# Performance work log

Measured on AMD Instinct MI355X. Metric: run time of the kernel, lower is better.

The kernel has to match this reference:

```python
import jax, jax.numpy as jnp
import numpy as np

SOS = 1
EOS = 2


def setup_inputs() -> dict:
    key = jax.random.key(0)
    ks = jax.random.split(key, 8)
    B, Z, C, E, H, V = 64, 512, 512, 1024, 1024, 32000
    sc = 0.05  # small init so tanh/sigmoid stay in a sane range
    return {
        "zs": jax.random.normal(ks[0], (B, Z), jnp.float32),
        "cs": jax.random.normal(ks[1], (B, C), jnp.float32),
        "emb": jax.random.normal(ks[2], (V, E), jnp.float32) * sc,
        "W_ih": jax.random.normal(ks[3], (3 * H, E), jnp.float32) * sc,
        "W_hh": jax.random.normal(ks[4], (3 * H, H), jnp.float32) * sc,
        "b_ih": jnp.zeros((3 * H,), jnp.float32),
        "b_hh": jnp.zeros((3 * H,), jnp.float32),
        "W_out": jax.random.normal(ks[5], (V, H), jnp.float32) * sc,
        "b_out": jnp.zeros((V,), jnp.float32),
        "max_utt_len": 32,
    }


def _gru_cell(x, h, W_ih, W_hh, b_ih, b_hh):
    # PyTorch GRU cell math (single layer)
    gi = x @ W_ih.T + b_ih              # [B, 3H]
    gh = h @ W_hh.T + b_hh              # [B, 3H]
    i_r, i_z, i_n = jnp.split(gi, 3, axis=-1)
    h_r, h_z, h_n = jnp.split(gh, 3, axis=-1)
    r = jax.nn.sigmoid(i_r + h_r)
    z = jax.nn.sigmoid(i_z + h_z)
    n = jnp.tanh(i_n + r * h_n)
    return (1.0 - z) * n + z * h


def reference(zs, cs, emb, W_ih, W_hh, b_ih, b_hh, W_out, b_out, max_utt_len):
    B = zs.shape[0]
    h0 = jnp.concatenate([zs, cs], axis=1)       # [B, H] initial hidden (zcs)
    x0 = emb[jnp.full((B,), SOS)]                # embedded SOS tokens [B, E]

    def step(carry, _):
        x, h = carry
        h = _gru_cell(x, h, W_ih, W_hh, b_ih, b_hh)
        logits = h @ W_out.T + b_out             # [B, V]
        tok = jnp.argmax(logits, axis=-1)        # greedy decode
        return (emb[tok], h), tok

    (_, _), toks = jax.lax.scan(step, (x0, h0), None, length=max_utt_len)
    resps = toks.T.astype(jnp.int64)             # [B, T]

    # resp_lens: index of first EOS (with EOS appended) + 1
    eos = jnp.concatenate([resps == EOS, jnp.ones((B, 1), bool)], axis=1)
    resp_lens = jnp.argmax(eos, axis=1).astype(jnp.int64) + 1
    return resps, resp_lens
```

## Files before the change

kernel.cpp:

```cpp
#include <hip/hip_runtime.h>
#include <hip/hip_bf16.h>
#include <float.h>

#define NB 64
#define HD 1024
#define H3 3072
#define NC6 6144
#define NV 32000
#define TSTEPS 32
#define LBLK 500
#define BML 512
#define NSLICE 8
#define NKT 16
#define MARGIN_COEF 0.010f
#define MARGIN_ABS  1e-3f
#define MAXCAND 1024

using bf16x8 = __attribute__((ext_vector_type(8))) short;
using f32x4  = __attribute__((ext_vector_type(4))) float;
using s16x4  = __attribute__((ext_vector_type(4))) short;

#define SWZ(row, bo) ((((bo) & ~127)) | (((bo) & 112) ^ (((row) & 7) << 4)) | ((bo) & 15))

__device__ __forceinline__ void gl_lds16(const void* g, void* l) {
    __builtin_amdgcn_global_load_lds(
        (const __attribute__((address_space(1))) void*)g,
        (__attribute__((address_space(3))) void*)l, 16, 0, 0);
}
__device__ __forceinline__ float sigmoidf_(float x) {
    return 1.0f / (1.0f + expf(-x));
}
__device__ __forceinline__ float dot4(float4 h, float4 w, float a) {
    return fmaf(h.w, w.w, fmaf(h.z, w.z, fmaf(h.y, w.y, fmaf(h.x, w.x, a))));
}
__device__ __forceinline__ short bf16bits(float x) {
    __hip_bfloat16 b = __float2bfloat16(x);
    return __builtin_bit_cast(short, b);
}
__device__ __forceinline__ float bf16val(short s) {
    __hip_bfloat16 b = __builtin_bit_cast(__hip_bfloat16, s);
    return __bfloat162float(b);
}
__device__ __forceinline__ unsigned ordbits(float v) {
    unsigned u = __float_as_uint(v);
    return (u & 0x80000000u) ? ~u : (u | 0x80000000u);
}

__global__ __launch_bounds__(256) void wsplit2_kernel(
    const float* __restrict__ Wih, const float* __restrict__ Whh,
    short* __restrict__ WihSp, short* __restrict__ WhhSp)
{
    int r = blockIdx.x;
    const float* src = (r < H3) ? &Wih[(size_t)r * HD] : &Whh[(size_t)(r - H3) * HD];
    char* dst = (char*)((r < H3) ? &WihSp[(size_t)r * 2048] : &WhhSp[(size_t)(r - H3) * 2048]);
    int k = threadIdx.x * 4;
    float4 v = *(const float4*)&src[k];
    float xs[4] = {v.x, v.y, v.z, v.w};
    s16x4 p1, p2;
    #pragma unroll
    for (int e = 0; e < 4; ++e) {
        short s1 = bf16bits(xs[e]);
        short s2 = bf16bits(xs[e] - bf16val(s1));
        p1[e] = s1; p2[e] = s2;
    }
    int bo = k * 2;
    *(s16x4*)(dst + SWZ(r, bo))        = p1;
    *(s16x4*)(dst + SWZ(r, 2048 + bo)) = p2;
}

__global__ __launch_bounds__(256) void wbf_kernel(const float* __restrict__ W,
                                                  short* __restrict__ Wbf,
                                                  float* __restrict__ wnorm)
{
    int r = blockIdx.x, tdx = threadIdx.x;
    float4 v = *(const float4*)&W[(size_t)r * HD + tdx * 4];
    s16x4 p;
    p[0] = bf16bits(v.x); p[1] = bf16bits(v.y);
    p[2] = bf16bits(v.z); p[3] = bf16bits(v.w);
    char* dst = (char*)(Wbf + (size_t)r * HD);
    *(s16x4*)(dst + SWZ(r, tdx * 8)) = p;
    float ss = v.x*v.x + v.y*v.y + v.z*v.z + v.w*v.w;
    #pragma unroll
    for (int off = 32; off; off >>= 1) ss += __shfl_xor(ss, off);
    __shared__ float red[4];
    if ((tdx & 63) == 0) red[tdx >> 6] = ss;
    __syncthreads();
    if (tdx == 0) wnorm[r] = sqrtf(red[0] + red[1] + red[2] + red[3]);
}

__global__ __launch_bounds__(256) void init_kernel(
    const float* __restrict__ zs, const float* __restrict__ cs,
    const float* __restrict__ emb,
    float4* __restrict__ ht4, short* __restrict__ Hsp, short* __restrict__ Xsp,
    float* __restrict__ hnorm, unsigned long long* __restrict__ best)
{
    int b = blockIdx.x;
    int kg = threadIdx.x;
    int j = kg * 4;
    float4 v;
    if (j < 512) v = *(const float4*)&zs[b * 512 + j];
    else         v = *(const float4*)&cs[b * 512 + (j - 512)];
    ht4[kg * NB + b] = v;
    float hs[4] = {v.x, v.y, v.z, v.w};
    s16x4 p1, p2;
    #pragma unroll
    for (int e = 0; e < 4; ++e) {
        short s1 = bf16bits(hs[e]);
        short s2 = bf16bits(hs[e] - bf16val(s1));
        p1[e] = s1; p2[e] = s2;
    }
    int bo = j * 2;
    char* hdst = (char*)(Hsp + (size_t)b * 2048);
    *(s16x4*)(hdst + SWZ(b, bo))        = p1;
    *(s16x4*)(hdst + SWZ(b, 2048 + bo)) = p2;

    float4 x = *(const float4*)&emb[HD + j];
    float xs[4] = {x.x, x.y, x.z, x.w};
    #pragma unroll
    for (int e = 0; e < 4; ++e) {
        short s1 = bf16bits(xs[e]);
        short s2 = bf16bits(xs[e] - bf16val(s1));
        p1[e] = s1; p2[e] = s2;
    }
    char* xdst = (char*)(Xsp + (size_t)b * 2048);
    *(s16x4*)(xdst + SWZ(b, bo))        = p1;
    *(s16x4*)(xdst + SWZ(b, 2048 + bo)) = p2;

    float ss = hs[0]*hs[0] + hs[1]*hs[1] + hs[2]*hs[2] + hs[3]*hs[3];
    #pragma unroll
    for (int off = 32; off; off >>= 1) ss += __shfl_xor(ss, off);
    __shared__ float red[4];
    if ((kg & 63) == 0) red[kg >> 6] = ss;
    __syncthreads();
    if (kg == 0) {
        hnorm[b] = sqrtf(red[0] + red[1] + red[2] + red[3]);
        best[b] = 0ull;
    }
}

__global__ __launch_bounds__(256, 2) void gates_mfma(
    const short* __restrict__ Xsp, const short* __restrict__ Hsp,
    const short* __restrict__ WihSp, const short* __restrict__ WhhSp,
    float* __restrict__ gpart)
{
    __shared__ __align__(16) char tile[2][16384];

    const int tid = threadIdx.x;
    const int wv = tid >> 6, l = tid & 63;
    int cg = blockIdx.x >> 2;
    int ks = blockIdx.x & 3;
    int c0 = cg * 64;
    bool isH = c0 >= H3;
    const short* __restrict__ Asrc = isH ? Hsp : Xsp;
    const short* __restrict__ Wsrc = isH ? WhhSp : WihSp;
    int wc0 = c0 - (isH ? H3 : 0);
    int k0 = ks * 1024;
    int ka0 = (k0 & 1023) + (((k0 >> 10) & 1) << 10);
    int kw0 = (k0 & 1023) + ((k0 >> 11) << 10);

    const short* srows[4];
    int lof[4];
    #pragma unroll
    for (int i = 0; i < 4; ++i) {
        int slot = i * 256 + tid;
        int row = slot >> 3;
        int kb  = (slot & 7) * 16;
        const short* g = (row < 64)
            ? (Asrc + (size_t)row * 2048 + ka0)
            : (Wsrc + (size_t)(wc0 + row - 64) * 2048 + kw0);
        srows[i] = g + (kb >> 1);
        lof[i] = slot * 16;
    }

    int a_off[4][2], b_off[2];
    #pragma unroll
    for (int m = 0; m < 4; ++m)
        #pragma unroll
        for (int kf = 0; kf < 2; ++kf) {
            int row = m * 16 + (l & 15);
            int kb = kf * 64 + (l >> 4) * 16;
            a_off[m][kf] = row * 128 + (kb ^ ((row & 7) << 4));
        }
    #pragma unroll
    for (int kf = 0; kf < 2; ++kf) {
        int row = 64 + wv * 16 + (l & 15);
        int kb = kf * 64 + (l >> 4) * 16;
        b_off[kf] = row * 128 + (kb ^ ((row & 7) << 4));
    }

    f32x4 acc[4] = {};

    #pragma unroll
    for (int i = 0; i < 4; ++i) gl_lds16(srows[i], tile[0] + lof[i]);
    __syncthreads();

    int cur = 0;
    #pragma unroll 1
    for (int kt = 0; kt < NKT; ++kt) {
        if (kt + 1 < NKT) {
            #pragma unroll
            for (int i = 0; i < 4; ++i)
                gl_lds16(srows[i] + (size_t)(kt + 1) * 64, tile[cur ^ 1] + lof[i]);
        }
        char* buf = tile[cur];
        #pragma unroll
        for (int kf = 0; kf < 2; ++kf) {
            bf16x8 bfrag = *(const bf16x8*)(buf + b_off[kf]);
            #pragma unroll
            for (int m = 0; m < 4; ++m) {
                bf16x8 afrag = *(const bf16x8*)(buf + a_off[m][kf]);
                acc[m] = __builtin_amdgcn_mfma_f32_16x16x32_bf16(afrag, bfrag, acc[m], 0, 0, 0);
            }
        }
        __syncthreads();
        cur ^= 1;
    }

    int colw = c0 + wv * 16 + (l & 15);
    #pragma unroll
    for (int m = 0; m < 4; ++m)
        #pragma unroll
        for (int j = 0; j < 4; ++j) {
            int row = m * 16 + (l >> 4) * 4 + j;
            gpart[(size_t)(ks * NB + row) * NC6 + colw] = acc[m][j];
        }
}

__global__ __launch_bounds__(256) void gru_fuse(
    const float* __restrict__ gpart,
    const float* __restrict__ bih, const float* __restrict__ bhh,
    float4* __restrict__ ht4, short* __restrict__ Hsp,
    float* __restrict__ hnorm, unsigned long long* __restrict__ best)
{
    int b = blockIdx.x;
    int kg = threadIdx.x;
    int j0 = kg * 4;
    float4 ir = {}, iz = {}, in_ = {}, hr = {}, hz = {}, hn = {};
    #pragma unroll
    for (int ks = 0; ks < 4; ++ks) {
        const float* g = gpart + (size_t)(ks * NB + b) * NC6;
        float4 a;
        a = *(const float4*)&g[j0];             ir.x+=a.x; ir.y+=a.y; ir.z+=a.z; ir.w+=a.w;
        a = *(const float4*)&g[HD + j0];        iz.x+=a.x; iz.y+=a.y; iz.z+=a.z; iz.w+=a.w;
        a = *(const float4*)&g[2*HD + j0];      in_.x+=a.x; in_.y+=a.y; in_.z+=a.z; in_.w+=a.w;
        a = *(const float4*)&g[H3 + j0];        hr.x+=a.x; hr.y+=a.y; hr.z+=a.z; hr.w+=a.w;
        a = *(const float4*)&g[H3 + HD + j0];   hz.x+=a.x; hz.y+=a.y; hz.z+=a.z; hz.w+=a.w;
        a = *(const float4*)&g[H3 + 2*HD + j0]; hn.x+=a.x; hn.y+=a.y; hn.z+=a.z; hn.w+=a.w;
    }
    float4 vbi0 = *(const float4*)&bih[j0];
    float4 vbi1 = *(const float4*)&bih[HD + j0];
    float4 vbi2 = *(const float4*)&bih[2*HD + j0];
    float4 vbh0 = *(const float4*)&bhh[j0];
    float4 vbh1 = *(const float4*)&bhh[HD + j0];
    float4 vbh2 = *(const float4*)&bhh[2*HD + j0];
    float4 hv = ht4[kg * NB + b];
    float irv[4] = {ir.x+vbi0.x, ir.y+vbi0.y, ir.z+vbi0.z, ir.w+vbi0.w};
    float izv[4] = {iz.x+vbi1.x, iz.y+vbi1.y, iz.z+vbi1.z, iz.w+vbi1.w};
    float inv[4] = {in_.x+vbi2.x, in_.y+vbi2.y, in_.z+vbi2.z, in_.w+vbi2.w};
    float hrv[4] = {hr.x+vbh0.x, hr.y+vbh0.y, hr.z+vbh0.z, hr.w+vbh0.w};
    float hzv[4] = {hz.x+vbh1.x, hz.y+vbh1.y, hz.z+vbh1.z, hz.w+vbh1.w};
    float hnv[4] = {hn.x+vbh2.x, hn.y+vbh2.y, hn.z+vbh2.z, hn.w+vbh2.w};
    float hvv[4] = {hv.x, hv.y, hv.z, hv.w};
    float o[4];
    #pragma unroll
    for (int u = 0; u < 4; ++u) {
        float r = sigmoidf_(irv[u] + hrv[u]);
        float z = sigmoidf_(izv[u] + hzv[u]);
        float n = tanhf(inv[u] + r * hnv[u]);
        o[u] = (1.0f - z) * n + z * hvv[u];
    }
    ht4[kg * NB + b] = make_float4(o[0], o[1], o[2], o[3]);

    s16x4 p1, p2;
    #pragma unroll
    for (int e = 0; e < 4; ++e) {
        short s1 = bf16bits(o[e]);
        short s2 = bf16bits(o[e] - bf16val(s1));
        p1[e] = s1; p2[e] = s2;
    }
    int bo = j0 * 2;
    char* hdst = (char*)(Hsp + (size_t)b * 2048);
    *(s16x4*)(hdst + SWZ(b, bo))        = p1;
    *(s16x4*)(hdst + SWZ(b, 2048 + bo)) = p2;

    float ss = o[0]*o[0] + o[1]*o[1] + o[2]*o[2] + o[3]*o[3];
    #pragma unroll
    for (int off = 32; off; off >>= 1) ss += __shfl_xor(ss, off);
    __shared__ float red[4];
    if ((kg & 63) == 0) red[kg >> 6] = ss;
    __syncthreads();
    if (kg == 0) {
        hnorm[b] = sqrtf(red[0] + red[1] + red[2] + red[3]);
        best[b] = 0ull;
    }
}

__global__ __launch_bounds__(256, 2) void logits_lb(
    const short* __restrict__ Hsp, const short* __restrict__ Wbf,
    const float* __restrict__ bout, const float* __restrict__ wnorm,
    const float* __restrict__ hnorm,
    float* __restrict__ lb, float* __restrict__ bmlow)
{
    __shared__ __align__(16) char tile[2][16384];
    __shared__ float smax[64][4];

    const int tid = threadIdx.x;
    const int wv = tid >> 6, l = tid & 63;
    const int blk = blockIdx.x;

    const short* srows[4];
    int lof[4];
    #pragma unroll
    for (int i = 0; i < 4; ++i) {
        int slot = i * 256 + tid;
        int row = slot >> 3;
        int kb  = (slot & 7) * 16;
        const short* g = (row < 64)
            ? (Hsp + (size_t)row * 2048)
            : (Wbf + ((size_t)(blk * 64 + (row - 64))) * HD);
        srows[i] = g + (kb >> 1);
        lof[i] = slot * 16;
    }

    int a_off[4][2], b_off[2];
    #pragma unroll
    for (int m = 0; m < 4; ++m)
        #pragma unroll
        for (int kf = 0; kf < 2; ++kf) {
            int row = m * 16 + (l & 15);
            int kb = kf * 64 + (l >> 4) * 16;
            a_off[m][kf] = row * 128 + (kb ^ ((row & 7) << 4));
        }
    #pragma unroll
    for (int kf = 0; kf < 2; ++kf) {
        int row = 64 + wv * 16 + (l & 15);
        int kb = kf * 64 + (l >> 4) * 16;
        b_off[kf] = row * 128 + (kb ^ ((row & 7) << 4));
    }

    f32x4 acc[4] = {};

    #pragma unroll
    for (int i = 0; i < 4; ++i) gl_lds16(srows[i], tile[0] + lof[i]);
    __syncthreads();

    int cur = 0;
    #pragma unroll 1
    for (int kt = 0; kt < NKT; ++kt) {
        if (kt + 1 < NKT) {
            #pragma unroll
            for (int i = 0; i < 4; ++i)
                gl_lds16(srows[i] + (size_t)(kt + 1) * 64, tile[cur ^ 1] + lof[i]);
        }
        char* buf = tile[cur];
        #pragma unroll
        for (int kf = 0; kf < 2; ++kf) {
            bf16x8 bfrag = *(const bf16x8*)(buf + b_off[kf]);
            #pragma unroll
            for (int m = 0; m < 4; ++m) {
                bf16x8 afrag = *(const bf16x8*)(buf + a_off[m][kf]);
                acc[m] = __builtin_amdgcn_mfma_f32_16x16x32_bf16(afrag, bfrag, acc[m], 0, 0, 0);
            }
        }
        __syncthreads();
        cur ^= 1;
    }

    int col = blk * 64 + wv * 16 + (l & 15);
    float bo = bout[col];
    float wn = wnorm[col];
    float selmax = -FLT_MAX;
    int pick = l & 15;
    #pragma unroll
    for (int m = 0; m < 4; ++m) {
        #pragma unroll
        for (int j = 0; j < 4; ++j) {
            int row = m * 16 + (l >> 4) * 4 + j;
            float lbv = acc[m][j] + bo;
            lb[(size_t)row * NV + col] = lbv;
            float low = lbv - (MARGIN_COEF * hnorm[row] * wn + MARGIN_ABS);
            #pragma unroll
            for (int mask = 1; mask <= 8; mask <<= 1)
                low = fmaxf(low, __shfl_xor(low, mask, 64));
            if (pick == m * 4 + j) selmax = low;
        }
    }
    int row = ((l & 15) >> 2) * 16 + (l >> 4) * 4 + (l & 3);
    smax[row][wv] = selmax;
    __syncthreads();
    if (wv == 0) {
        float v = fmaxf(fmaxf(smax[l][0], smax[l][1]), fmaxf(smax[l][2], smax[l][3]));
        bmlow[(size_t)l * BML + blk] = v;
    }
}

__global__ __launch_bounds__(256) void select2_kernel(
    const float* __restrict__ lb, const float* __restrict__ wnorm,
    const float* __restrict__ hnorm, const float* __restrict__ bmlow,
    const float* __restrict__ Wout, const float* __restrict__ bout,
    const float4* __restrict__ ht4,
    unsigned long long* __restrict__ best)
{
    int b = blockIdx.x >> 3, slice = blockIdx.x & 7;
    int tid = threadIdx.x, wv = tid >> 6;
    const float* lbr = lb + (size_t)b * NV;
    float coef = MARGIN_COEF * hnorm[b];

    __shared__ int scount;
    __shared__ int cand[MAXCAND];
    __shared__ float tred[4];
    if (tid == 0) scount = 0;

    float tv = -FLT_MAX;
    for (int i = tid; i < LBLK; i += 256) tv = fmaxf(tv, bmlow[(size_t)b * BML + i]);
    #pragma unroll
    for (int off = 32; off; off >>= 1) tv = fmaxf(tv, __shfl_xor(tv, off));
    if ((tid & 63) == 0) tred[wv] = tv;
    __syncthreads();
    float tb = fmaxf(fmaxf(tred[0], tred[1]), fmaxf(tred[2], tred[3]));

    int c0 = slice * (NV / NSLICE);
    for (int c = c0 + tid; c < c0 + NV / NSLICE; c += 256) {
        if (lbr[c] + (coef * wnorm[c] + MARGIN_ABS) >= tb) {
            int s = atomicAdd(&scount, 1);
            if (s < MAXCAND) cand[s] = c;
        }
    }
    __syncthreads();
    int n = scount < MAXCAND ? scount : MAXCAND;
    if (n == 0) return;

    float4 h4 = ht4[tid * NB + b];
    __shared__ float rsum[4];
    for (int s = 0; s < n; ++s) {
        int c = cand[s];
        float4 w4 = *(const float4*)&Wout[(size_t)c * HD + tid * 4];
        float p = dot4(h4, w4, 0.0f);
        #pragma unroll
        for (int off = 32; off; off >>= 1) p += __shfl_xor(p, off);
        if ((tid & 63) == 0) rsum[wv] = p;
        __syncthreads();
        if (tid == 0) {
            float tot = rsum[0] + rsum[1] + rsum[2] + rsum[3] + bout[c];
            unsigned long long key =
                ((unsigned long long)ordbits(tot) << 32) | (unsigned)(~c);
            atomicMax(&best[b], key);
        }
        __syncthreads();
    }
}

__global__ __launch_bounds__(256) void gather_kernel(
    const unsigned long long* __restrict__ best,
    const float* __restrict__ emb, int* __restrict__ resps, int t,
    short* __restrict__ Xsp)
{
    int b = blockIdx.x, tid = threadIdx.x;
    int c = ~(unsigned)(best[b] & 0xFFFFFFFFull);
    if (tid == 0) resps[b * TSTEPS + t] = c;
    int k = tid * 4;
    float4 e = *(const float4*)&emb[(size_t)c * HD + k];
    float xs[4] = {e.x, e.y, e.z, e.w};
    s16x4 p1, p2;
    #pragma unroll
    for (int u = 0; u < 4; ++u) {
        short s1 = bf16bits(xs[u]);
        short s2 = bf16bits(xs[u] - bf16val(s1));
        p1[u] = s1; p2[u] = s2;
    }
    int bo = k * 2;
    char* xdst = (char*)(Xsp + (size_t)b * 2048);
    *(s16x4*)(xdst + SWZ(b, bo))        = p1;
    *(s16x4*)(xdst + SWZ(b, 2048 + bo)) = p2;
}

__global__ void resp_lens_kernel(const int* __restrict__ resps, int* __restrict__ lens)
{
    int b = threadIdx.x;
    if (b >= NB) return;
    int len = TSTEPS + 1;
    for (int t = TSTEPS - 1; t >= 0; t--)
        if (resps[b * TSTEPS + t] == 2) len = t + 1;
    lens[b] = len;
}

extern "C" void kernel_launch(void* const* d_in, const int* in_sizes, int n_in,
                              void* d_out, int out_size, void* d_ws, size_t ws_size,
                              hipStream_t stream) {
    const float* zs   = (const float*)d_in[0];
    const float* cs   = (const float*)d_in[1];
    const float* emb  = (const float*)d_in[2];
    const float* Wih  = (const float*)d_in[3];
    const float* Whh  = (const float*)d_in[4];
    const float* bih  = (const float*)d_in[5];
    const float* bhh  = (const float*)d_in[6];
    const float* Wout = (const float*)d_in[7];
    const float* bout = (const float*)d_in[8];
    int* out = (int*)d_out;

    char* ws = (char*)d_ws;
    float4* ht4  = (float4*)ws; ws += (size_t)256 * NB * 16;
    float*  gpart = (float*)ws; ws += (size_t)4 * NB * NC6 * 4;
    short*  Hsp  = (short*)ws;  ws += (size_t)NB * 2048 * 2;
    short*  Xsp  = (short*)ws;  ws += (size_t)NB * 2048 * 2;
    float*  wnorm = (float*)ws; ws += (size_t)NV * 4;
    float*  hnorm = (float*)ws; ws += 256;
    float*  bmlow = (float*)ws; ws += (size_t)NB * BML * 4;
    unsigned long long* best = (unsigned long long*)ws; ws += NB * 8;
    float*  lb   = (float*)ws;  ws += (size_t)NB * NV * 4;
    short*  Wbf  = (short*)ws;  ws += (size_t)NV * HD * 2;
    short*  WihSp = (short*)ws; ws += (size_t)H3 * 2048 * 2;
    short*  WhhSp = (short*)ws; ws += (size_t)H3 * 2048 * 2;

    wsplit2_kernel<<<NC6, 256, 0, stream>>>(Wih, Whh, WihSp, WhhSp);
    wbf_kernel<<<NV, 256, 0, stream>>>(Wout, Wbf, wnorm);
    init_kernel<<<NB, 256, 0, stream>>>(zs, cs, emb, ht4, Hsp, Xsp, hnorm, best);
    for (int t = 0; t < TSTEPS; t++) {
        gates_mfma<<<96 * 4, 256, 0, stream>>>(Xsp, Hsp, WihSp, WhhSp, gpart);
        gru_fuse<<<NB, 256, 0, stream>>>(gpart, bih, bhh, ht4, Hsp, hnorm, best);
        logits_lb<<<LBLK, 256, 0, stream>>>(Hsp, Wbf, bout, wnorm, hnorm, lb, bmlow);
        select2_kernel<<<NB * NSLICE, 256, 0, stream>>>(lb, wnorm, hnorm, bmlow,
                                                        Wout, bout, ht4, best);
        gather_kernel<<<NB, 256, 0, stream>>>(best, emb, out, t, Xsp);
    }
    resp_lens_kernel<<<1, 64, 0, stream>>>(out, out + NB * TSTEPS);
}
```

Measured before the change: 1.599 ms.

## Deepen MFMA load pipeline to 3 stages and fuse gather into select

The two MFMA GEMM kernels move from a double-buffered LDS tile with two barriers per k-step to a four-slot ring that prefetches two tiles ahead. Each step now has a single explicit vmcnt wait plus barrier, so global loads get more time to overlap with compute. Separately, the per-step gather kernel is removed. The last select block for each batch row, found by an atomic done counter, reads the winning token, writes the response and builds the next split-bf16 embedding input. This trades an extra LDS footprint per block and some fence/atomic overhead for fewer launches and less load stall.

```diff
diff --git a/kernel.cpp b/kernel.cpp
--- a/kernel.cpp
+++ b/kernel.cpp
@@ -46,6 +46,12 @@
     return (u & 0x80000000u) ? ~u : (u | 0x80000000u);
 }
 
+#define WAIT_BARRIER(kt) do { \
+    if ((kt) < NKT - 2)       asm volatile("s_waitcnt vmcnt(8)\ns_barrier" ::: "memory"); \
+    else if ((kt) == NKT - 2) asm volatile("s_waitcnt vmcnt(4)\ns_barrier" ::: "memory"); \
+    else                      asm volatile("s_waitcnt vmcnt(0)\ns_barrier" ::: "memory"); \
+} while (0)
+
 __global__ __launch_bounds__(256) void wsplit2_kernel(
     const float* __restrict__ Wih, const float* __restrict__ Whh,
     short* __restrict__ WihSp, short* __restrict__ WhhSp)
@@ -92,7 +98,8 @@
     const float* __restrict__ zs, const float* __restrict__ cs,
     const float* __restrict__ emb,
     float4* __restrict__ ht4, short* __restrict__ Hsp, short* __restrict__ Xsp,
-    float* __restrict__ hnorm, unsigned long long* __restrict__ best)
+    float* __restrict__ hnorm, unsigned long long* __restrict__ best,
+    int* __restrict__ done)
 {
     int b = blockIdx.x;
     int kg = threadIdx.x;
@@ -135,6 +142,7 @@
     if (kg == 0) {
         hnorm[b] = sqrtf(red[0] + red[1] + red[2] + red[3]);
         best[b] = 0ull;
+        done[b] = 0;
     }
 }
 
@@ -143,7 +151,7 @@
     const short* __restrict__ WihSp, const short* __restrict__ WhhSp,
     float* __restrict__ gpart)
 {
-    __shared__ __align__(16) char tile[2][16384];
+    __shared__ __align__(16) char tile[4][16384];
 
     const int tid = threadIdx.x;
     const int wv = tid >> 6, l = tid & 63;
@@ -192,17 +200,18 @@
 
     #pragma unroll
     for (int i = 0; i < 4; ++i) gl_lds16(srows[i], tile[0] + lof[i]);
-    __syncthreads();
-
-    int cur = 0;
+    #pragma unroll
+    for (int i = 0; i < 4; ++i) gl_lds16(srows[i] + 64, tile[1] + lof[i]);
+
     #pragma unroll 1
     for (int kt = 0; kt < NKT; ++kt) {
-        if (kt + 1 < NKT) {
+        if (kt + 2 < NKT) {
             #pragma unroll
             for (int i = 0; i < 4; ++i)
-                gl_lds16(srows[i] + (size_t)(kt + 1) * 64, tile[cur ^ 1] + lof[i]);
-        }
-        char* buf = tile[cur];
+                gl_lds16(srows[i] + (size_t)(kt + 2) * 64, tile[(kt + 2) & 3] + lof[i]);
+        }
+        WAIT_BARRIER(kt);
+        const char* buf = tile[kt & 3];
         #pragma unroll
         for (int kf = 0; kf < 2; ++kf) {
             bf16x8 bfrag = *(const bf16x8*)(buf + b_off[kf]);
@@ -212,8 +221,6 @@
                 acc[m] = __builtin_amdgcn_mfma_f32_16x16x32_bf16(afrag, bfrag, acc[m], 0, 0, 0);
             }
         }
-        __syncthreads();
-        cur ^= 1;
     }
 
     int colw = c0 + wv * 16 + (l & 15);
@@ -230,7 +237,8 @@
     const float* __restrict__ gpart,
     const float* __restrict__ bih, const float* __restrict__ bhh,
     float4* __restrict__ ht4, short* __restrict__ Hsp,
-    float* __restrict__ hnorm, unsigned long long* __restrict__ best)
+    float* __restrict__ hnorm, unsigned long long* __restrict__ best,
+    int* __restrict__ done)
 {
     int b = blockIdx.x;
     int kg = threadIdx.x;
@@ -292,6 +300,7 @@
     if (kg == 0) {
         hnorm[b] = sqrtf(red[0] + red[1] + red[2] + red[3]);
         best[b] = 0ull;
+        done[b] = 0;
     }
 }
 
@@ -301,7 +310,7 @@
     const float* __restrict__ hnorm,
     float* __restrict__ lb, float* __restrict__ bmlow)
 {
-    __shared__ __align__(16) char tile[2][16384];
+    __shared__ __align__(16) char tile[4][16384];
     __shared__ float smax[64][4];
 
     const int tid = threadIdx.x;
@@ -342,17 +351,18 @@
 
     #pragma unroll
     for (int i = 0; i < 4; ++i) gl_lds16(srows[i], tile[0] + lof[i]);
-    __syncthreads();
-
-    int cur = 0;
+    #pragma unroll
+    for (int i = 0; i < 4; ++i) gl_lds16(srows[i] + 64, tile[1] + lof[i]);
+
     #pragma unroll 1
     for (int kt = 0; kt < NKT; ++kt) {
-        if (kt + 1 < NKT) {
+        if (kt + 2 < NKT) {
             #pragma unroll
             for (int i = 0; i < 4; ++i)
-                gl_lds16(srows[i] + (size_t)(kt + 1) * 64, tile[cur ^ 1] + lof[i]);
-        }
-        char* buf = tile[cur];
+                gl_lds16(srows[i] + (size_t)(kt + 2) * 64, tile[(kt + 2) & 3] + lof[i]);
+        }
+        WAIT_BARRIER(kt);
+        const char* buf = tile[kt & 3];
         #pragma unroll
         for (int kf = 0; kf < 2; ++kf) {
             bf16x8 bfrag = *(const bf16x8*)(buf + b_off[kf]);
@@ -362,8 +372,6 @@
                 acc[m] = __builtin_amdgcn_mfma_f32_16x16x32_bf16(afrag, bfrag, acc[m], 0, 0, 0);
             }
         }
-        __syncthreads();
-        cur ^= 1;
     }
 
     int col = blk * 64 + wv * 16 + (l & 15);
@@ -398,8 +406,9 @@
     const float* __restrict__ lb, const float* __restrict__ wnorm,
     const float* __restrict__ hnorm, const float* __restrict__ bmlow,
     const float* __restrict__ Wout, const float* __restrict__ bout,
-    const float4* __restrict__ ht4,
-    unsigned long long* __restrict__ best)
+    const float4* __restrict__ ht4, const float* __restrict__ emb,
+    unsigned long long* __restrict__ best, int* __restrict__ done,
+    int* __restrict__ resps, int t, short* __restrict__ Xsp)
 {
     int b = blockIdx.x >> 3, slice = blockIdx.x & 7;
     int tid = threadIdx.x, wv = tid >> 6;
@@ -409,6 +418,8 @@
     __shared__ int scount;
     __shared__ int cand[MAXCAND];
     __shared__ float tred[4];
+    __shared__ int lastflag;
+    __shared__ unsigned long long kbest;
     if (tid == 0) scount = 0;
 
     float tv = -FLT_MAX;
@@ -428,7 +439,6 @@
     }
     __syncthreads();
     int n = scount < MAXCAND ? scount : MAXCAND;
-    if (n == 0) return;
 
     float4 h4 = ht4[tid * NB + b];
     __shared__ float rsum[4];
@@ -448,30 +458,36 @@
         }
         __syncthreads();
     }
-}
-
-__global__ __launch_bounds__(256) void gather_kernel(
-    const unsigned long long* __restrict__ best,
-    const float* __restrict__ emb, int* __restrict__ resps, int t,
-    short* __restrict__ Xsp)
-{
-    int b = blockIdx.x, tid = threadIdx.x;
-    int c = ~(unsigned)(best[b] & 0xFFFFFFFFull);
-    if (tid == 0) resps[b * TSTEPS + t] = c;
-    int k = tid * 4;
-    float4 e = *(const float4*)&emb[(size_t)c * HD + k];
-    float xs[4] = {e.x, e.y, e.z, e.w};
-    s16x4 p1, p2;
-    #pragma unroll
-    for (int u = 0; u < 4; ++u) {
-        short s1 = bf16bits(xs[u]);
-        short s2 = bf16bits(xs[u] - bf16val(s1));
-        p1[u] = s1; p2[u] = s2;
-    }
-    int bo = k * 2;
-    char* xdst = (char*)(Xsp + (size_t)b * 2048);
-    *(s16x4*)(xdst + SWZ(b, bo))        = p1;
-    *(s16x4*)(xdst + SWZ(b, 2048 + bo)) = p2;
+
+    __threadfence();
+    if (tid == 0) {
+        int old = atomicAdd(&done[b], 1);
+        lastflag = (old == NSLICE - 1);
+    }
+    __syncthreads();
+    if (lastflag) {
+        if (tid == 0) {
+            __threadfence();
+            kbest = atomicMax(&best[b], 0ull);
+        }
+        __syncthreads();
+        int tok = ~(unsigned)(kbest & 0xFFFFFFFFull);
+        if (tid == 0) resps[b * TSTEPS + t] = tok;
+        int k = tid * 4;
+        float4 e = *(const float4*)&emb[(size_t)tok * HD + k];
+        float xs[4] = {e.x, e.y, e.z, e.w};
+        s16x4 p1, p2;
+        #pragma unroll
+        for (int u = 0; u < 4; ++u) {
+            short s1 = bf16bits(xs[u]);
+            short s2 = bf16bits(xs[u] - bf16val(s1));
+            p1[u] = s1; p2[u] = s2;
+        }
+        int bo = k * 2;
+        char* xdst = (char*)(Xsp + (size_t)b * 2048);
+        *(s16x4*)(xdst + SWZ(b, bo))        = p1;
+        *(s16x4*)(xdst + SWZ(b, 2048 + bo)) = p2;
+    }
 }
 
 __global__ void resp_lens_kernel(const int* __restrict__ resps, int* __restrict__ lens)
@@ -507,6 +523,7 @@
     float*  hnorm = (float*)ws; ws += 256;
     float*  bmlow = (float*)ws; ws += (size_t)NB * BML * 4;
     unsigned long long* best = (unsigned long long*)ws; ws += NB * 8;
+    int*    done = (int*)ws;    ws += 256;
     float*  lb   = (float*)ws;  ws += (size_t)NB * NV * 4;
     short*  Wbf  = (short*)ws;  ws += (size_t)NV * HD * 2;
     short*  WihSp = (short*)ws; ws += (size_t)H3 * 2048 * 2;
@@ -514,14 +531,13 @@
 
     wsplit2_kernel<<<NC6, 256, 0, stream>>>(Wih, Whh, WihSp, WhhSp);
     wbf_kernel<<<NV, 256, 0, stream>>>(Wout, Wbf, wnorm);
-    init_kernel<<<NB, 256, 0, stream>>>(zs, cs, emb, ht4, Hsp, Xsp, hnorm, best);
+    init_kernel<<<NB, 256, 0, stream>>>(zs, cs, emb, ht4, Hsp, Xsp, hnorm, best, done);
     for (int t = 0; t < TSTEPS; t++) {
         gates_mfma<<<96 * 4, 256, 0, stream>>>(Xsp, Hsp, WihSp, WhhSp, gpart);
-        gru_fuse<<<NB, 256, 0, stream>>>(gpart, bih, bhh, ht4, Hsp, hnorm, best);
+        gru_fuse<<<NB, 256, 0, stream>>>(gpart, bih, bhh, ht4, Hsp, hnorm, best, done);
         logits_lb<<<LBLK, 256, 0, stream>>>(Hsp, Wbf, bout, wnorm, hnorm, lb, bmlow);
-        select2_kernel<<<NB * NSLICE, 256, 0, stream>>>(lb, wnorm, hnorm, bmlow,
-                                                        Wout, bout, ht4, best);
-        gather_kernel<<<NB, 256, 0, stream>>>(best, emb, out, t, Xsp);
+        select2_kernel<<<NB * NSLICE, 256, 0, stream>>>(lb, wnorm, hnorm, bmlow, Wout, bout,
+                                                        ht4, emb, best, done, out, t, Xsp);
     }
     resp_lens_kernel<<<1, 64, 0, stream>>>(out, out + NB * TSTEPS);
 }
```

New measurement: 2.826 ms. 76.8% more time.

## Fuse embedding gather into gates GEMM via presplit embedding table

Applied to the files above, without the earlier changes.

Precomputes a bf16 hi/lo split of the whole embedding table once. The gates kernel then reads the previous step's argmax token from a per-step best array and loads the embedding rows directly, so the per-step gather kernel goes away. The best-key array becomes per-timestep, which also removes the per-step reset, and a final kernel extracts tokens and lengths. The trade-off is an extra one-time conversion pass over the 32000x1024 embedding table, plus an extra dependent token load inside the GEMM address setup.

```diff
diff --git a/kernel.cpp b/kernel.cpp
--- a/kernel.cpp
+++ b/kernel.cpp
@@ -88,6 +88,25 @@
     if (tdx == 0) wnorm[r] = sqrtf(red[0] + red[1] + red[2] + red[3]);
 }
 
+__global__ __launch_bounds__(256) void embsplit_kernel(const float* __restrict__ emb,
+                                                       short* __restrict__ EmbSp)
+{
+    int r = blockIdx.x;
+    int k = threadIdx.x * 4;
+    float4 v = *(const float4*)&emb[(size_t)r * HD + k];
+    float xs[4] = {v.x, v.y, v.z, v.w};
+    s16x4 p1, p2;
+    #pragma unroll
+    for (int e = 0; e < 4; ++e) {
+        short s1 = bf16bits(xs[e]);
+        short s2 = bf16bits(xs[e] - bf16val(s1));
+        p1[e] = s1; p2[e] = s2;
+    }
+    short* dst = EmbSp + (size_t)r * 2048;
+    *(s16x4*)(dst + k)        = p1;
+    *(s16x4*)(dst + 1024 + k) = p2;
+}
+
 __global__ __launch_bounds__(256) void init_kernel(
     const float* __restrict__ zs, const float* __restrict__ cs,
     const float* __restrict__ emb,
@@ -122,9 +141,11 @@
         short s2 = bf16bits(xs[e] - bf16val(s1));
         p1[e] = s1; p2[e] = s2;
     }
-    char* xdst = (char*)(Xsp + (size_t)b * 2048);
-    *(s16x4*)(xdst + SWZ(b, bo))        = p1;
-    *(s16x4*)(xdst + SWZ(b, 2048 + bo)) = p2;
+    short* xdst = Xsp + (size_t)b * 2048;
+    *(s16x4*)(xdst + j)        = p1;
+    *(s16x4*)(xdst + 1024 + j) = p2;
+
+    if (kg < TSTEPS) best[kg * NB + b] = 0ull;
 
     float ss = hs[0]*hs[0] + hs[1]*hs[1] + hs[2]*hs[2] + hs[3]*hs[3];
     #pragma unroll
@@ -132,15 +153,14 @@
     __shared__ float red[4];
     if ((kg & 63) == 0) red[kg >> 6] = ss;
     __syncthreads();
-    if (kg == 0) {
-        hnorm[b] = sqrtf(red[0] + red[1] + red[2] + red[3]);
-        best[b] = 0ull;
-    }
+    if (kg == 0) hnorm[b] = sqrtf(red[0] + red[1] + red[2] + red[3]);
 }
 
 __global__ __launch_bounds__(256, 2) void gates_mfma(
-    const short* __restrict__ Xsp, const short* __restrict__ Hsp,
+    const short* __restrict__ Xsp, const short* __restrict__ EmbSp,
+    const short* __restrict__ Hsp,
     const short* __restrict__ WihSp, const short* __restrict__ WhhSp,
+    const unsigned long long* __restrict__ bprev, int use_tok,
     float* __restrict__ gpart)
 {
     __shared__ __align__(16) char tile[2][16384];
@@ -151,7 +171,6 @@
     int ks = blockIdx.x & 3;
     int c0 = cg * 64;
     bool isH = c0 >= H3;
-    const short* __restrict__ Asrc = isH ? Hsp : Xsp;
     const short* __restrict__ Wsrc = isH ? WhhSp : WihSp;
     int wc0 = c0 - (isH ? H3 : 0);
     int k0 = ks * 1024;
@@ -165,10 +184,25 @@
         int slot = i * 256 + tid;
         int row = slot >> 3;
         int kb  = (slot & 7) * 16;
-        const short* g = (row < 64)
-            ? (Asrc + (size_t)row * 2048 + ka0)
-            : (Wsrc + (size_t)(wc0 + row - 64) * 2048 + kw0);
-        srows[i] = g + (kb >> 1);
+        const short* g;
+        if (row < 64) {
+            if (isH) {
+                g = Hsp + (size_t)row * 2048 + ka0 + (kb >> 1);
+            } else {
+                const short* abase;
+                if (use_tok) {
+                    unsigned tok = ~(unsigned)(bprev[row] & 0xFFFFFFFFull);
+                    abase = EmbSp + (size_t)tok * 2048;
+                } else {
+                    abase = Xsp + (size_t)row * 2048;
+                }
+                int skb = kb ^ ((row & 7) << 4);
+                g = abase + ka0 + (skb >> 1);
+            }
+        } else {
+            g = Wsrc + (size_t)(wc0 + row - 64) * 2048 + kw0 + (kb >> 1);
+        }
+        srows[i] = g;
         lof[i] = slot * 16;
     }
 
@@ -230,7 +264,7 @@
     const float* __restrict__ gpart,
     const float* __restrict__ bih, const float* __restrict__ bhh,
     float4* __restrict__ ht4, short* __restrict__ Hsp,
-    float* __restrict__ hnorm, unsigned long long* __restrict__ best)
+    float* __restrict__ hnorm)
 {
     int b = blockIdx.x;
     int kg = threadIdx.x;
@@ -289,10 +323,7 @@
     __shared__ float red[4];
     if ((kg & 63) == 0) red[kg >> 6] = ss;
     __syncthreads();
-    if (kg == 0) {
-        hnorm[b] = sqrtf(red[0] + red[1] + red[2] + red[3]);
-        best[b] = 0ull;
-    }
+    if (kg == 0) hnorm[b] = sqrtf(red[0] + red[1] + red[2] + red[3]);
 }
 
 __global__ __launch_bounds__(256, 2) void logits_lb(
@@ -450,38 +481,18 @@
     }
 }
 
-__global__ __launch_bounds__(256) void gather_kernel(
-    const unsigned long long* __restrict__ best,
-    const float* __restrict__ emb, int* __restrict__ resps, int t,
-    short* __restrict__ Xsp)
-{
-    int b = blockIdx.x, tid = threadIdx.x;
-    int c = ~(unsigned)(best[b] & 0xFFFFFFFFull);
-    if (tid == 0) resps[b * TSTEPS + t] = c;
-    int k = tid * 4;
-    float4 e = *(const float4*)&emb[(size_t)c * HD + k];
-    float xs[4] = {e.x, e.y, e.z, e.w};
-    s16x4 p1, p2;
-    #pragma unroll
-    for (int u = 0; u < 4; ++u) {
-        short s1 = bf16bits(xs[u]);
-        short s2 = bf16bits(xs[u] - bf16val(s1));
-        p1[u] = s1; p2[u] = s2;
-    }
-    int bo = k * 2;
-    char* xdst = (char*)(Xsp + (size_t)b * 2048);
-    *(s16x4*)(xdst + SWZ(b, bo))        = p1;
-    *(s16x4*)(xdst + SWZ(b, 2048 + bo)) = p2;
-}
-
-__global__ void resp_lens_kernel(const int* __restrict__ resps, int* __restrict__ lens)
+__global__ void resp_extract_kernel(const unsigned long long* __restrict__ best,
+                                    int* __restrict__ out)
 {
     int b = threadIdx.x;
     if (b >= NB) return;
     int len = TSTEPS + 1;
-    for (int t = TSTEPS - 1; t >= 0; t--)
-        if (resps[b * TSTEPS + t] == 2) len = t + 1;
-    lens[b] = len;
+    for (int t = TSTEPS - 1; t >= 0; t--) {
+        int tok = ~(unsigned)(best[(size_t)t * NB + b] & 0xFFFFFFFFull);
+        out[b * TSTEPS + t] = tok;
+        if (tok == 2) len = t + 1;
+    }
+    out[NB * TSTEPS + b] = len;
 }
 
 extern "C" void kernel_launch(void* const* d_in, const int* in_sizes, int n_in,
@@ -506,22 +517,25 @@
     float*  wnorm = (float*)ws; ws += (size_t)NV * 4;
     float*  hnorm = (float*)ws; ws += 256;
     float*  bmlow = (float*)ws; ws += (size_t)NB * BML * 4;
-    unsigned long long* best = (unsigned long long*)ws; ws += NB * 8;
+    unsigned long long* best = (unsigned long long*)ws; ws += (size_t)TSTEPS * NB * 8;
     float*  lb   = (float*)ws;  ws += (size_t)NB * NV * 4;
     short*  Wbf  = (short*)ws;  ws += (size_t)NV * HD * 2;
     short*  WihSp = (short*)ws; ws += (size_t)H3 * 2048 * 2;
     short*  WhhSp = (short*)ws; ws += (size_t)H3 * 2048 * 2;
+    short*  EmbSp = (short*)ws; ws += (size_t)NV * 2048 * 2;
 
     wsplit2_kernel<<<NC6, 256, 0, stream>>>(Wih, Whh, WihSp, WhhSp);
     wbf_kernel<<<NV, 256, 0, stream>>>(Wout, Wbf, wnorm);
+    embsplit_kernel<<<NV, 256, 0, stream>>>(emb, EmbSp);
     init_kernel<<<NB, 256, 0, stream>>>(zs, cs, emb, ht4, Hsp, Xsp, hnorm, best);
     for (int t = 0; t < TSTEPS; t++) {
-        gates_mfma<<<96 * 4, 256, 0, stream>>>(Xsp, Hsp, WihSp, WhhSp, gpart);
-        gru_fuse<<<NB, 256, 0, stream>>>(gpart, bih, bhh, ht4, Hsp, hnorm, best);
+        gates_mfma<<<96 * 4, 256, 0, stream>>>(Xsp, EmbSp, Hsp, WihSp, WhhSp,
+                                               (t > 0) ? (best + (size_t)(t - 1) * NB) : best,
+                                               (t > 0) ? 1 : 0, gpart);
+        gru_fuse<<<NB, 256, 0, stream>>>(gpart, bih, bhh, ht4, Hsp, hnorm);
         logits_lb<<<LBLK, 256, 0, stream>>>(Hsp, Wbf, bout, wnorm, hnorm, lb, bmlow);
         select2_kernel<<<NB * NSLICE, 256, 0, stream>>>(lb, wnorm, hnorm, bmlow,
-                                                        Wout, bout, ht4, best);
-        gather_kernel<<<NB, 256, 0, stream>>>(best, emb, out, t, Xsp);
-    }
-    resp_lens_kernel<<<1, 64, 0, stream>>>(out, out + NB * TSTEPS);
-}
+                                                        Wout, bout, ht4, best + (size_t)t * NB);
+    }
+    resp_extract_kernel<<<1, 64, 0, stream>>>(best, out);
+}
```

After: 1.683 ms. 5.2% more time.

## Prune candidate scan with per-block upper bounds and fuse select with gather

Applied to the files above, without the earlier changes.

logits_lb now also records a per-block maximum of the upper bound (lb plus margin), so the selection kernel only scans the 64-column blocks whose upper bound reaches the threshold instead of all 32000 lower-bound entries. Selection and the embedding gather are merged into one kernel per batch row, which tracks the best token locally. This removes the best-array atomics and one launch per step. The cost is extra shuffles and stores in the logits kernel. The fused kernel runs only 64 blocks, and the surviving blocks are scanned serially using just 64 threads.

```diff
diff --git a/kernel.cpp b/kernel.cpp
--- a/kernel.cpp
+++ b/kernel.cpp
@@ -10,7 +10,6 @@
 #define TSTEPS 32
 #define LBLK 500
 #define BML 512
-#define NSLICE 8
 #define NKT 16
 #define MARGIN_COEF 0.010f
 #define MARGIN_ABS  1e-3f
@@ -40,10 +39,6 @@
 __device__ __forceinline__ float bf16val(short s) {
     __hip_bfloat16 b = __builtin_bit_cast(__hip_bfloat16, s);
     return __bfloat162float(b);
-}
-__device__ __forceinline__ unsigned ordbits(float v) {
-    unsigned u = __float_as_uint(v);
-    return (u & 0x80000000u) ? ~u : (u | 0x80000000u);
 }
 
 __global__ __launch_bounds__(256) void wsplit2_kernel(
@@ -92,7 +87,7 @@
     const float* __restrict__ zs, const float* __restrict__ cs,
     const float* __restrict__ emb,
     float4* __restrict__ ht4, short* __restrict__ Hsp, short* __restrict__ Xsp,
-    float* __restrict__ hnorm, unsigned long long* __restrict__ best)
+    float* __restrict__ hnorm)
 {
     int b = blockIdx.x;
     int kg = threadIdx.x;
@@ -132,10 +127,7 @@
     __shared__ float red[4];
     if ((kg & 63) == 0) red[kg >> 6] = ss;
     __syncthreads();
-    if (kg == 0) {
-        hnorm[b] = sqrtf(red[0] + red[1] + red[2] + red[3]);
-        best[b] = 0ull;
-    }
+    if (kg == 0) hnorm[b] = sqrtf(red[0] + red[1] + red[2] + red[3]);
 }
 
 __global__ __launch_bounds__(256, 2) void gates_mfma(
@@ -230,7 +222,7 @@
     const float* __restrict__ gpart,
     const float* __restrict__ bih, const float* __restrict__ bhh,
     float4* __restrict__ ht4, short* __restrict__ Hsp,
-    float* __restrict__ hnorm, unsigned long long* __restrict__ best)
+    float* __restrict__ hnorm)
 {
     int b = blockIdx.x;
     int kg = threadIdx.x;
@@ -289,20 +281,18 @@
     __shared__ float red[4];
     if ((kg & 63) == 0) red[kg >> 6] = ss;
     __syncthreads();
-    if (kg == 0) {
-        hnorm[b] = sqrtf(red[0] + red[1] + red[2] + red[3]);
-        best[b] = 0ull;
-    }
+    if (kg == 0) hnorm[b] = sqrtf(red[0] + red[1] + red[2] + red[3]);
 }
 
 __global__ __launch_bounds__(256, 2) void logits_lb(
     const short* __restrict__ Hsp, const short* __restrict__ Wbf,
     const float* __restrict__ bout, const float* __restrict__ wnorm,
     const float* __restrict__ hnorm,
-    float* __restrict__ lb, float* __restrict__ bmlow)
+    float* __restrict__ lb, float* __restrict__ bmlow, float* __restrict__ bmhigh)
 {
     __shared__ __align__(16) char tile[2][16384];
     __shared__ float smax[64][4];
+    __shared__ float shigh[64][4];
 
     const int tid = threadIdx.x;
     const int wv = tid >> 6, l = tid & 63;
@@ -369,7 +359,7 @@
     int col = blk * 64 + wv * 16 + (l & 15);
     float bo = bout[col];
     float wn = wnorm[col];
-    float selmax = -FLT_MAX;
+    float selmax = -FLT_MAX, selhigh = -FLT_MAX;
     int pick = l & 15;
     #pragma unroll
     for (int m = 0; m < 4; ++m) {
@@ -378,38 +368,47 @@
             int row = m * 16 + (l >> 4) * 4 + j;
             float lbv = acc[m][j] + bo;
             lb[(size_t)row * NV + col] = lbv;
-            float low = lbv - (MARGIN_COEF * hnorm[row] * wn + MARGIN_ABS);
+            float marg = MARGIN_COEF * hnorm[row] * wn + MARGIN_ABS;
+            float low = lbv - marg;
+            float high = lbv + marg;
             #pragma unroll
-            for (int mask = 1; mask <= 8; mask <<= 1)
-                low = fmaxf(low, __shfl_xor(low, mask, 64));
-            if (pick == m * 4 + j) selmax = low;
+            for (int mask = 1; mask <= 8; mask <<= 1) {
+                low  = fmaxf(low,  __shfl_xor(low,  mask, 64));
+                high = fmaxf(high, __shfl_xor(high, mask, 64));
+            }
+            if (pick == m * 4 + j) { selmax = low; selhigh = high; }
         }
     }
     int row = ((l & 15) >> 2) * 16 + (l >> 4) * 4 + (l & 3);
     smax[row][wv] = selmax;
+    shigh[row][wv] = selhigh;
     __syncthreads();
     if (wv == 0) {
         float v = fmaxf(fmaxf(smax[l][0], smax[l][1]), fmaxf(smax[l][2], smax[l][3]));
+        float h = fmaxf(fmaxf(shigh[l][0], shigh[l][1]), fmaxf(shigh[l][2], shigh[l][3]));
         bmlow[(size_t)l * BML + blk] = v;
-    }
-}
-
-__global__ __launch_bounds__(256) void select2_kernel(
+        bmhigh[(size_t)l * BML + blk] = h;
+    }
+}
+
+__global__ __launch_bounds__(256) void select_gather(
     const float* __restrict__ lb, const float* __restrict__ wnorm,
-    const float* __restrict__ hnorm, const float* __restrict__ bmlow,
+    const float* __restrict__ hnorm,
+    const float* __restrict__ bmlow, const float* __restrict__ bmhigh,
     const float* __restrict__ Wout, const float* __restrict__ bout,
-    const float4* __restrict__ ht4,
-    unsigned long long* __restrict__ best)
-{
-    int b = blockIdx.x >> 3, slice = blockIdx.x & 7;
+    const float4* __restrict__ ht4, const float* __restrict__ emb,
+    int* __restrict__ resps, int t, short* __restrict__ Xsp)
+{
+    int b = blockIdx.x;
     int tid = threadIdx.x, wv = tid >> 6;
-    const float* lbr = lb + (size_t)b * NV;
     float coef = MARGIN_COEF * hnorm[b];
 
-    __shared__ int scount;
+    __shared__ float tred[4];
+    __shared__ float rsum[4];
+    __shared__ int qcount, scount, stok;
+    __shared__ int qblk[BML];
     __shared__ int cand[MAXCAND];
-    __shared__ float tred[4];
-    if (tid == 0) scount = 0;
+    if (tid == 0) { qcount = 0; scount = 0; }
 
     float tv = -FLT_MAX;
     for (int i = tid; i < LBLK; i += 256) tv = fmaxf(tv, bmlow[(size_t)b * BML + i]);
@@ -419,19 +418,30 @@
     __syncthreads();
     float tb = fmaxf(fmaxf(tred[0], tred[1]), fmaxf(tred[2], tred[3]));
 
-    int c0 = slice * (NV / NSLICE);
-    for (int c = c0 + tid; c < c0 + NV / NSLICE; c += 256) {
-        if (lbr[c] + (coef * wnorm[c] + MARGIN_ABS) >= tb) {
-            int s = atomicAdd(&scount, 1);
-            if (s < MAXCAND) cand[s] = c;
+    for (int i = tid; i < LBLK; i += 256) {
+        if (bmhigh[(size_t)b * BML + i] >= tb) {
+            int s = atomicAdd(&qcount, 1);
+            qblk[s] = i;
+        }
+    }
+    __syncthreads();
+    int qn = qcount;
+
+    const float* lbr = lb + (size_t)b * NV;
+    for (int q = 0; q < qn; ++q) {
+        if (tid < 64) {
+            int c = qblk[q] * 64 + tid;
+            if (lbr[c] + (coef * wnorm[c] + MARGIN_ABS) >= tb) {
+                int s = atomicAdd(&scount, 1);
+                if (s < MAXCAND) cand[s] = c;
+            }
         }
     }
     __syncthreads();
     int n = scount < MAXCAND ? scount : MAXCAND;
-    if (n == 0) return;
 
     float4 h4 = ht4[tid * NB + b];
-    __shared__ float rsum[4];
+    float bv = -FLT_MAX; int bc = 0x7fffffff;
     for (int s = 0; s < n; ++s) {
         int c = cand[s];
         float4 w4 = *(const float4*)&Wout[(size_t)c * HD + tid * 4];
@@ -442,24 +452,16 @@
         __syncthreads();
         if (tid == 0) {
             float tot = rsum[0] + rsum[1] + rsum[2] + rsum[3] + bout[c];
-            unsigned long long key =
-                ((unsigned long long)ordbits(tot) << 32) | (unsigned)(~c);
-            atomicMax(&best[b], key);
+            if (tot > bv || (tot == bv && c < bc)) { bv = tot; bc = c; }
         }
         __syncthreads();
     }
-}
-
-__global__ __launch_bounds__(256) void gather_kernel(
-    const unsigned long long* __restrict__ best,
-    const float* __restrict__ emb, int* __restrict__ resps, int t,
-    short* __restrict__ Xsp)
-{
-    int b = blockIdx.x, tid = threadIdx.x;
-    int c = ~(unsigned)(best[b] & 0xFFFFFFFFull);
-    if (tid == 0) resps[b * TSTEPS + t] = c;
+    if (tid == 0) { resps[b * TSTEPS + t] = bc; stok = bc; }
+    __syncthreads();
+
+    int tok = stok;
     int k = tid * 4;
-    float4 e = *(const float4*)&emb[(size_t)c * HD + k];
+    float4 e = *(const float4*)&emb[(size_t)tok * HD + k];
     float xs[4] = {e.x, e.y, e.z, e.w};
     s16x4 p1, p2;
     #pragma unroll
@@ -506,7 +508,7 @@
     float*  wnorm = (float*)ws; ws += (size_t)NV * 4;
     float*  hnorm = (float*)ws; ws += 256;
     float*  bmlow = (float*)ws; ws += (size_t)NB * BML * 4;
-    unsigned long long* best = (unsigned long long*)ws; ws += NB * 8;
+    float*  bmhigh = (float*)ws; ws += (size_t)NB * BML * 4;
     float*  lb   = (float*)ws;  ws += (size_t)NB * NV * 4;
     short*  Wbf  = (short*)ws;  ws += (size_t)NV * HD * 2;
     short*  WihSp = (short*)ws; ws += (size_t)H3 * 2048 * 2;
@@ -514,14 +516,13 @@
 
     wsplit2_kernel<<<NC6, 256, 0, stream>>>(Wih, Whh, WihSp, WhhSp);
     wbf_kernel<<<NV, 256, 0, stream>>>(Wout, Wbf, wnorm);
-    init_kernel<<<NB, 256, 0, stream>>>(zs, cs, emb, ht4, Hsp, Xsp, hnorm, best);
+    init_kernel<<<NB, 256, 0, stream>>>(zs, cs, emb, ht4, Hsp, Xsp, hnorm);
     for (int t = 0; t < TSTEPS; t++) {
         gates_mfma<<<96 * 4, 256, 0, stream>>>(Xsp, Hsp, WihSp, WhhSp, gpart);
-        gru_fuse<<<NB, 256, 0, stream>>>(gpart, bih, bhh, ht4, Hsp, hnorm, best);
-        logits_lb<<<LBLK, 256, 0, stream>>>(Hsp, Wbf, bout, wnorm, hnorm, lb, bmlow);
-        select2_kernel<<<NB * NSLICE, 256, 0, stream>>>(lb, wnorm, hnorm, bmlow,
-                                                        Wout, bout, ht4, best);
-        gather_kernel<<<NB, 256, 0, stream>>>(best, emb, out, t, Xsp);
+        gru_fuse<<<NB, 256, 0, stream>>>(gpart, bih, bhh, ht4, Hsp, hnorm);
+        logits_lb<<<LBLK, 256, 0, stream>>>(Hsp, Wbf, bout, wnorm, hnorm, lb, bmlow, bmhigh);
+        select_gather<<<NB, 256, 0, stream>>>(lb, wnorm, hnorm, bmlow, bmhigh,
+                                              Wout, bout, ht4, emb, out, t, Xsp);
     }
     resp_lens_kernel<<<1, 64, 0, stream>>>(out, out + NB * TSTEPS);
 }
```

New measurement: 2.882 ms. +80.2%, slower.
